# Performance work log

Hardware: AMD Instinct MI355X
Metric: run time of the kernel (lower is better)

Reference implementation:

```python
import jax, jax.numpy as jnp
import numpy as np

H = 1024  # hidden_size


def _cell(x, W, b):
    # x: [S, B, D_in]; W: [4H, D_in]; b: [4H]
    # One big batched matmul over all timesteps (no recurrence exists).
    gates = jnp.einsum('sbd,gd->sbg', x, W) + b  # [S, B, 4H]
    i, f, g, o = jnp.split(gates, 4, axis=-1)
    i = jax.nn.sigmoid(i)
    g = jnp.tanh(g)
    o = jax.nn.sigmoid(o)
    c = i * g
    h = o * jnp.tanh(c)
    return h, c


def setup_inputs() -> dict:
    key = jax.random.key(0)
    ks = jax.random.split(key, 9)
    S, B, D = 2048, 8, 1024
    s = 1.0 / np.sqrt(D)
    s2 = 1.0 / np.sqrt(2 * H)
    return {
        'x': jax.random.normal(ks[0], (S, B, D), dtype=jnp.float32),
        'W_f0': jax.random.uniform(ks[1], (4 * H, D), jnp.float32, -s, s),
        'b_f0': jax.random.uniform(ks[2], (4 * H,), jnp.float32, -s, s),
        'W_b0': jax.random.uniform(ks[3], (4 * H, D), jnp.float32, -s, s),
        'b_b0': jax.random.uniform(ks[4], (4 * H,), jnp.float32, -s, s),
        'W_f1': jax.random.uniform(ks[5], (4 * H, 2 * H), jnp.float32, -s2, s2),
        'b_f1': jax.random.uniform(ks[6], (4 * H,), jnp.float32, -s2, s2),
        'W_b1': jax.random.uniform(ks[7], (4 * H, 2 * H), jnp.float32, -s2, s2),
        'b_b1': jax.random.uniform(ks[8], (4 * H,), jnp.float32, -s2, s2),
    }


def reference(x, W_f0, b_f0, W_b0, b_b0, W_f1, b_f1, W_b1, b_b1):
    out = x
    h_ns, c_ns = [], []
    for (Wf, bf, Wb, bb) in [(W_f0, b_f0, W_b0, b_b0), (W_f1, b_f1, W_b1, b_b1)]:
        h_f, c_f = _cell(out, Wf, bf)  # forward direction
        h_b, c_b = _cell(out, Wb, bb)  # backward direction (same per-t math)
        out = jnp.concatenate([h_f, h_b], axis=-1)  # [S, B, 2H]
        # forward final state is at t = S-1; backward final state at t = 0
        h_ns += [h_f[-1], h_b[0]]
        c_ns += [c_f[-1], c_b[0]]
    h_n = jnp.stack(h_ns, axis=0)  # [num_layers*2, B, H]
    c_n = jnp.stack(c_ns, axis=0)
    return out, h_n, c_n
```

## Files before the change

### kernel.cpp

```cpp
#include <hip/hip_runtime.h>
#include <hip/hip_bf16.h>

#define S_LEN 2048
#define BATCH 8
#define HID   1024
#define NP    3072
#define MROWS 16384

using bf16x8 = __attribute__((ext_vector_type(8))) short;
using f32x4  = __attribute__((ext_vector_type(4))) float;

__device__ __forceinline__ unsigned short f2b(float f) {
  unsigned int u = __builtin_bit_cast(unsigned int, f);
  u += 0x7fffu + ((u >> 16) & 1u);
  return (unsigned short)(u >> 16);
}

__device__ __forceinline__ void load_lds16(const void* g, void* l) {
  __builtin_amdgcn_global_load_lds(
      (const __attribute__((address_space(1))) void*)g,
      (__attribute__((address_space(3))) void*)(unsigned int)(unsigned long long)l,
      16, 0, 0);
}

__global__ void cvt_f32_bf16(const float* __restrict__ in,
                             unsigned short* __restrict__ out, int n4) {
  int i = blockIdx.x * blockDim.x + threadIdx.x;
  if (i >= n4) return;
  const float4 v = reinterpret_cast<const float4*>(in)[i];
  ushort4 u;
  u.x = f2b(v.x); u.y = f2b(v.y); u.z = f2b(v.z); u.w = f2b(v.w);
  reinterpret_cast<ushort4*>(out)[i] = u;
}

__global__ void permute_w(const float* __restrict__ W,
                          unsigned short* __restrict__ Wp, int K) {
  long i = ((long)blockIdx.x * blockDim.x + threadIdx.x) * 4;
  int np = (int)(i / K);
  if (np >= NP) return;
  int k0 = (int)(i % K);
  int chunk = np / 48, rem = np % 48;
  int g3 = rem >> 4, hl = rem & 15;
  int og = (g3 == 0) ? 0 : (g3 == 1) ? 2 : 3;
  int n  = og * 1024 + chunk * 16 + hl;
  const float4 v = *reinterpret_cast<const float4*>(W + (long)n * K + k0);
  ushort4 u;
  u.x = f2b(v.x); u.y = f2b(v.y); u.z = f2b(v.z); u.w = f2b(v.w);
  *reinterpret_cast<ushort4*>(Wp + i) = u;
}

__global__ void permute_b(const float* __restrict__ b, float* __restrict__ bp) {
  int np = blockIdx.x * blockDim.x + threadIdx.x;
  if (np >= NP) return;
  int chunk = np / 48, rem = np % 48;
  int g3 = rem >> 4, hl = rem & 15;
  int og = (g3 == 0) ? 0 : (g3 == 1) ? 2 : 3;
  bp[np] = b[og * 1024 + chunk * 16 + hl];
}

template <int MODE>
__global__ void __launch_bounds__(256, 2)
lstm_gemm(const unsigned short* __restrict__ A,
          const unsigned short* __restrict__ WpF,
          const unsigned short* __restrict__ WpB,
          const float* __restrict__ bpF, const float* __restrict__ bpB,
          int K,
          unsigned short* __restrict__ out_bf, float* __restrict__ out_f,
          float* __restrict__ hn, float* __restrict__ cn) {
  const int dir = blockIdx.z;
  const unsigned short* __restrict__ Wp = dir ? WpB : WpF;
  const float* __restrict__ bp = dir ? bpB : bpF;
  const int bm = blockIdx.y;
  const int bn = blockIdx.x;

  __shared__ __align__(16) unsigned short Abuf[128 * 64];
  __shared__ __align__(16) unsigned short Bbuf[96 * 64];

  const int tid  = threadIdx.x;
  const int wid  = tid >> 6;
  const int lane = tid & 63;
  const int wm   = wid >> 1;
  const int wn   = wid & 1;

  f32x4 acc[4][3];
  const f32x4 zero = {0.f, 0.f, 0.f, 0.f};
#pragma unroll
  for (int i = 0; i < 4; ++i)
#pragma unroll
    for (int j = 0; j < 3; ++j) acc[i][j] = zero;

  const long a_base_row = (long)bm * 128;
  const long b_base_row = (long)bn * 96;
  const int  kt_count   = K >> 6;
  const long krow_bytes = (long)K * 2;

  for (int kt = 0; kt < kt_count; ++kt) {
    const long kbyte = (long)kt * 128;
#pragma unroll
    for (int it = 0; it < 4; ++it) {
      const int base = (it * 4 + wid) * 1024;
      const int p    = base + lane * 16;
      const int row  = p >> 7;
      const int colb = (p & 127) ^ ((row & 7) << 4);
      const char* src = (const char*)A + (a_base_row + row) * krow_bytes + kbyte + colb;
      load_lds16(src, (char*)Abuf + base);
    }
#pragma unroll
    for (int it = 0; it < 3; ++it) {
      const int base = (it * 4 + wid) * 1024;
      const int p    = base + lane * 16;
      const int row  = p >> 7;
      const int colb = (p & 127) ^ ((row & 7) << 4);
      const char* src = (const char*)Wp + (b_base_row + row) * krow_bytes + kbyte + colb;
      load_lds16(src, (char*)Bbuf + base);
    }
    asm volatile("s_waitcnt vmcnt(0)" ::: "memory");
    __syncthreads();

#pragma unroll
    for (int kb = 0; kb < 2; ++kb) {
      bf16x8 af[4];
      bf16x8 bfr[3];
#pragma unroll
      for (int mf = 0; mf < 4; ++mf) {
        const int row = wm * 64 + mf * 16 + (lane & 15);
        int byte = row * 128 + kb * 64 + ((lane >> 4) * 16);
        byte ^= (row & 7) << 4;
        af[mf] = *(const bf16x8*)((const char*)Abuf + byte);
      }
#pragma unroll
      for (int nf = 0; nf < 3; ++nf) {
        const int row = wn * 48 + nf * 16 + (lane & 15);
        int byte = row * 128 + kb * 64 + ((lane >> 4) * 16);
        byte ^= (row & 7) << 4;
        bfr[nf] = *(const bf16x8*)((const char*)Bbuf + byte);
      }
#pragma unroll
      for (int mf = 0; mf < 4; ++mf)
#pragma unroll
        for (int nf = 0; nf < 3; ++nf)
          acc[mf][nf] = __builtin_amdgcn_mfma_f32_16x16x32_bf16(
              af[mf], bfr[nf], acc[mf][nf], 0, 0, 0);
    }
    __syncthreads();
  }

  const int col    = lane & 15;
  const int chunk  = bn * 2 + wn;
  const int h      = chunk * 16 + col;
  const int outcol = dir * HID + h;
  const float bi = bp[chunk * 48 + col];
  const float bg = bp[chunk * 48 + 16 + col];
  const float bo = bp[chunk * 48 + 32 + col];
  const int Lidx = MODE * 2 + dir;

#pragma unroll
  for (int mf = 0; mf < 4; ++mf) {
#pragma unroll
    for (int r = 0; r < 4; ++r) {
      const int m = bm * 128 + wm * 64 + mf * 16 + (lane >> 4) * 4 + r;
      const float iv = acc[mf][0][r] + bi;
      const float gv = acc[mf][1][r] + bg;
      const float ov = acc[mf][2][r] + bo;
      const float is = 1.f / (1.f + __expf(-iv));
      const float gt = tanhf(gv);
      const float os = 1.f / (1.f + __expf(-ov));
      const float c  = is * gt;
      const float hv = os * tanhf(c);
      if (MODE == 0) {
        out_bf[(long)m * 2048 + outcol] = f2b(hv);
      } else {
        out_f[(long)m * 2048 + outcol] = hv;
      }
      const bool wst = (dir == 0) ? (m >= (S_LEN - 1) * BATCH) : (m < BATCH);
      if (wst) {
        const int b = (dir == 0) ? (m - (S_LEN - 1) * BATCH) : m;
        hn[((long)Lidx * BATCH + b) * HID + h] = hv;
        cn[((long)Lidx * BATCH + b) * HID + h] = c;
      }
    }
  }
}

extern "C" void kernel_launch(void* const* d_in, const int* in_sizes, int n_in,
                              void* d_out, int out_size, void* d_ws, size_t ws_size,
                              hipStream_t stream) {
  const float* x    = (const float*)d_in[0];
  const float* W_f0 = (const float*)d_in[1];
  const float* b_f0 = (const float*)d_in[2];
  const float* W_b0 = (const float*)d_in[3];
  const float* b_b0 = (const float*)d_in[4];
  const float* W_f1 = (const float*)d_in[5];
  const float* b_f1 = (const float*)d_in[6];
  const float* W_b1 = (const float*)d_in[7];
  const float* b_b1 = (const float*)d_in[8];

  float* out = (float*)d_out;
  float* hn  = out + (long)MROWS * 2048;
  float* cn  = hn + 4 * BATCH * HID;

  unsigned short* x_bf  = (unsigned short*)d_ws;
  unsigned short* out1  = x_bf + (long)MROWS * 1024;
  unsigned short* wp_f0 = out1 + (long)MROWS * 2048;
  unsigned short* wp_b0 = wp_f0 + (long)NP * 1024;
  unsigned short* wp_f1 = wp_b0 + (long)NP * 1024;
  unsigned short* wp_b1 = wp_f1 + (long)NP * 2048;
  float* bp_f0 = (float*)(wp_b1 + (long)NP * 2048);
  float* bp_b0 = bp_f0 + NP;
  float* bp_f1 = bp_b0 + NP;
  float* bp_b1 = bp_f1 + NP;

  cvt_f32_bf16<<<16384, 256, 0, stream>>>(x, x_bf, MROWS * 1024 / 4);
  permute_w<<<3072, 256, 0, stream>>>(W_f0, wp_f0, 1024);
  permute_w<<<3072, 256, 0, stream>>>(W_b0, wp_b0, 1024);
  permute_w<<<6144, 256, 0, stream>>>(W_f1, wp_f1, 2048);
  permute_w<<<6144, 256, 0, stream>>>(W_b1, wp_b1, 2048);
  permute_b<<<12, 256, 0, stream>>>(b_f0, bp_f0);
  permute_b<<<12, 256, 0, stream>>>(b_b0, bp_b0);
  permute_b<<<12, 256, 0, stream>>>(b_f1, bp_f1);
  permute_b<<<12, 256, 0, stream>>>(b_b1, bp_b1);

  dim3 grid(NP / 96, MROWS / 128, 2);
  lstm_gemm<0><<<grid, 256, 0, stream>>>(x_bf, wp_f0, wp_b0, bp_f0, bp_b0, 1024,
                                         out1, nullptr, hn, cn);
  lstm_gemm<1><<<grid, 256, 0, stream>>>(out1, wp_f1, wp_b1, bp_f1, bp_b1, 2048,
                                         nullptr, out, hn, cn);
}
```

Baseline: 666.3 us.

## Rewrite LSTM GEMM as 512-thread 128x384 tile with 4-stage LDS pipeline

The GEMM kernel moves from 256-thread 128x96 tiles with single-buffered LDS and a full vmcnt(0) wait each k-step to 512-thread 128x384 tiles. These use a 128KB LDS ring of four half-k stages, prefetched ahead with global_load_lds and interleaved with MFMA phases that raise wave priority via s_setprio. The goal is to hide global-load latency and increase reuse of each A tile across more gate columns. In exchange each block holds 24 accumulators per thread, uses many more barriers, and occupancy drops to about one block per CU because of the LDS footprint.

Measured after the change: 808.4 us. 1.21x slower.

```diff
diff --git a/kernel.cpp b/kernel.cpp
--- a/kernel.cpp
+++ b/kernel.cpp
@@ -22,6 +22,9 @@
       (__attribute__((address_space(3))) void*)(unsigned int)(unsigned long long)l,
       16, 0, 0);
 }
+
+#define MEMFENCE asm volatile("" ::: "memory")
+#define BARRIER  do { MEMFENCE; __builtin_amdgcn_s_barrier(); MEMFENCE; } while (0)
 
 __global__ void cvt_f32_bf16(const float* __restrict__ in,
                              unsigned short* __restrict__ out, int n4) {
@@ -59,7 +62,7 @@
 }
 
 template <int MODE>
-__global__ void __launch_bounds__(256, 2)
+__global__ void __launch_bounds__(512, 2)
 lstm_gemm(const unsigned short* __restrict__ A,
           const unsigned short* __restrict__ WpF,
           const unsigned short* __restrict__ WpB,
@@ -67,116 +70,150 @@
           int K,
           unsigned short* __restrict__ out_bf, float* __restrict__ out_f,
           float* __restrict__ hn, float* __restrict__ cn) {
+  __shared__ __align__(16) char lds[131072];
+
   const int dir = blockIdx.z;
   const unsigned short* __restrict__ Wp = dir ? WpB : WpF;
   const float* __restrict__ bp = dir ? bpB : bpF;
   const int bm = blockIdx.y;
   const int bn = blockIdx.x;
 
-  __shared__ __align__(16) unsigned short Abuf[128 * 64];
-  __shared__ __align__(16) unsigned short Bbuf[96 * 64];
-
   const int tid  = threadIdx.x;
   const int wid  = tid >> 6;
   const int lane = tid & 63;
-  const int wm   = wid >> 1;
-  const int wn   = wid & 1;
-
-  f32x4 acc[4][3];
+  const int wm   = wid >> 2;
+  const int wn   = wid & 3;
+
+  const int  nt = K >> 6;
+  const long K2 = (long)K * 2;
+
+  const int srow  = tid >> 3;
+  const int scolb = (((tid & 7) ^ (srow & 7)) << 4);
+  const char* Asrc = (const char*)A  + ((long)bm * 128 + srow) * K2 + scolb;
+  const char* Bsrc = (const char*)Wp + ((long)bn * 384 + srow) * K2 + scolb;
+  char* ldsw = lds + wid * 1024;
+
+  const int co0 = (((lane >> 4) << 4)) ^ ((lane & 7) << 4);
+  const int co1 = (64 + ((lane >> 4) << 4)) ^ ((lane & 7) << 4);
+  const int arow_off  = (lane & 15) * 128;
+  const int bbase_off = 8192 + (wn & 1) * 12288 + (lane & 15) * 128;
+
+  f32x4 acc[4][6];
   const f32x4 zero = {0.f, 0.f, 0.f, 0.f};
 #pragma unroll
   for (int i = 0; i < 4; ++i)
 #pragma unroll
-    for (int j = 0; j < 3; ++j) acc[i][j] = zero;
-
-  const long a_base_row = (long)bm * 128;
-  const long b_base_row = (long)bn * 96;
-  const int  kt_count   = K >> 6;
-  const long krow_bytes = (long)K * 2;
-
-  for (int kt = 0; kt < kt_count; ++kt) {
-    const long kbyte = (long)kt * 128;
-#pragma unroll
-    for (int it = 0; it < 4; ++it) {
-      const int base = (it * 4 + wid) * 1024;
-      const int p    = base + lane * 16;
-      const int row  = p >> 7;
-      const int colb = (p & 127) ^ ((row & 7) << 4);
-      const char* src = (const char*)A + (a_base_row + row) * krow_bytes + kbyte + colb;
-      load_lds16(src, (char*)Abuf + base);
+    for (int j = 0; j < 6; ++j) acc[i][j] = zero;
+
+  auto STAGE = [&](int s) {
+    if (s < 2 * nt) {
+      const long off = (long)(s >> 1) * 128;
+      const long h   = (long)(s & 1);
+      char* d = ldsw + (s & 3) * 32768;
+      load_lds16(Asrc + h * 64 * K2 + off,            d);
+      load_lds16(Bsrc + (h * 192      ) * K2 + off,   d + 8192);
+      load_lds16(Bsrc + (h * 192 +  64) * K2 + off,   d + 16384);
+      load_lds16(Bsrc + (h * 192 + 128) * K2 + off,   d + 24576);
     }
-#pragma unroll
-    for (int it = 0; it < 3; ++it) {
-      const int base = (it * 4 + wid) * 1024;
-      const int p    = base + lane * 16;
-      const int row  = p >> 7;
-      const int colb = (p & 127) ^ ((row & 7) << 4);
-      const char* src = (const char*)Wp + (b_base_row + row) * krow_bytes + kbyte + colb;
-      load_lds16(src, (char*)Bbuf + base);
+  };
+
+  STAGE(0); STAGE(1); STAGE(2); STAGE(3);
+  asm volatile("s_waitcnt vmcnt(8)" ::: "memory");
+  BARRIER;
+
+#define MFMA_ROW(mf, areg)                                                   \
+  do {                                                                       \
+    __builtin_amdgcn_s_setprio(1);                                           \
+    _Pragma("unroll")                                                        \
+    for (int nf = 0; nf < 6; ++nf) {                                         \
+      acc[mf][nf] = __builtin_amdgcn_mfma_f32_16x16x32_bf16(                 \
+          areg[0], b0[nf], acc[mf][nf], 0, 0, 0);                            \
+      acc[mf][nf] = __builtin_amdgcn_mfma_f32_16x16x32_bf16(                 \
+          areg[1], b1[nf], acc[mf][nf], 0, 0, 0);                            \
+    }                                                                        \
+    __builtin_amdgcn_s_setprio(0);                                           \
+  } while (0)
+
+  for (int t = 0; t < nt; ++t) {
+    const char* bufA = lds + ((2 * t + wm)        & 3) * 32768 + arow_off;
+    const char* bufB = lds + ((2 * t + (wn >> 1)) & 3) * 32768 + bbase_off;
+
+    bf16x8 b0[6], b1[6], a0[2], a1[2], a2[2], a3[2];
+
+#pragma unroll
+    for (int nf = 0; nf < 6; ++nf) {
+      b0[nf] = *(const bf16x8*)(bufB + nf * 2048 + co0);
+      b1[nf] = *(const bf16x8*)(bufB + nf * 2048 + co1);
     }
-    asm volatile("s_waitcnt vmcnt(0)" ::: "memory");
-    __syncthreads();
-
-#pragma unroll
-    for (int kb = 0; kb < 2; ++kb) {
-      bf16x8 af[4];
-      bf16x8 bfr[3];
-#pragma unroll
-      for (int mf = 0; mf < 4; ++mf) {
-        const int row = wm * 64 + mf * 16 + (lane & 15);
-        int byte = row * 128 + kb * 64 + ((lane >> 4) * 16);
-        byte ^= (row & 7) << 4;
-        af[mf] = *(const bf16x8*)((const char*)Abuf + byte);
-      }
-#pragma unroll
-      for (int nf = 0; nf < 3; ++nf) {
-        const int row = wn * 48 + nf * 16 + (lane & 15);
-        int byte = row * 128 + kb * 64 + ((lane >> 4) * 16);
-        byte ^= (row & 7) << 4;
-        bfr[nf] = *(const bf16x8*)((const char*)Bbuf + byte);
-      }
-#pragma unroll
-      for (int mf = 0; mf < 4; ++mf)
-#pragma unroll
-        for (int nf = 0; nf < 3; ++nf)
-          acc[mf][nf] = __builtin_amdgcn_mfma_f32_16x16x32_bf16(
-              af[mf], bfr[nf], acc[mf][nf], 0, 0, 0);
-    }
-    __syncthreads();
+    a0[0] = *(const bf16x8*)(bufA + co0);
+    a0[1] = *(const bf16x8*)(bufA + co1);
+    BARRIER;
+    asm volatile("s_waitcnt lgkmcnt(0)" ::: "memory");
+    MFMA_ROW(0, a0);
+    BARRIER;
+
+    a1[0] = *(const bf16x8*)(bufA + 2048 + co0);
+    a1[1] = *(const bf16x8*)(bufA + 2048 + co1);
+    a2[0] = *(const bf16x8*)(bufA + 4096 + co0);
+    a2[1] = *(const bf16x8*)(bufA + 4096 + co1);
+    a3[0] = *(const bf16x8*)(bufA + 6144 + co0);
+    a3[1] = *(const bf16x8*)(bufA + 6144 + co1);
+    BARRIER;
+    asm volatile("s_waitcnt lgkmcnt(0)" ::: "memory");
+    MFMA_ROW(1, a1);
+    BARRIER;
+
+    STAGE(2 * t + 4);
+    BARRIER;
+    MFMA_ROW(2, a2);
+    BARRIER;
+
+    STAGE(2 * t + 5);
+    BARRIER;
+    MFMA_ROW(3, a3);
+    if (t < nt - 2) { asm volatile("s_waitcnt vmcnt(8)" ::: "memory"); }
+    else            { asm volatile("s_waitcnt vmcnt(0)" ::: "memory"); }
+    BARRIER;
   }
+#undef MFMA_ROW
 
   const int col    = lane & 15;
-  const int chunk  = bn * 2 + wn;
-  const int h      = chunk * 16 + col;
-  const int outcol = dir * HID + h;
-  const float bi = bp[chunk * 48 + col];
-  const float bg = bp[chunk * 48 + 16 + col];
-  const float bo = bp[chunk * 48 + 32 + col];
-  const int Lidx = MODE * 2 + dir;
-
-#pragma unroll
-  for (int mf = 0; mf < 4; ++mf) {
-#pragma unroll
-    for (int r = 0; r < 4; ++r) {
-      const int m = bm * 128 + wm * 64 + mf * 16 + (lane >> 4) * 4 + r;
-      const float iv = acc[mf][0][r] + bi;
-      const float gv = acc[mf][1][r] + bg;
-      const float ov = acc[mf][2][r] + bo;
-      const float is = 1.f / (1.f + __expf(-iv));
-      const float gt = tanhf(gv);
-      const float os = 1.f / (1.f + __expf(-ov));
-      const float c  = is * gt;
-      const float hv = os * tanhf(c);
-      if (MODE == 0) {
-        out_bf[(long)m * 2048 + outcol] = f2b(hv);
-      } else {
-        out_f[(long)m * 2048 + outcol] = hv;
-      }
-      const bool wst = (dir == 0) ? (m >= (S_LEN - 1) * BATCH) : (m < BATCH);
-      if (wst) {
-        const int b = (dir == 0) ? (m - (S_LEN - 1) * BATCH) : m;
-        hn[((long)Lidx * BATCH + b) * HID + h] = hv;
-        cn[((long)Lidx * BATCH + b) * HID + h] = c;
+  const int rbase  = (lane >> 4) * 4;
+  const int chunk0 = bn * 8 + wn * 2;
+  const int Lidx   = MODE * 2 + dir;
+
+#pragma unroll
+  for (int hg = 0; hg < 2; ++hg) {
+    const int chunk  = chunk0 + hg;
+    const int h      = chunk * 16 + col;
+    const int outcol = dir * HID + h;
+    const float bi = bp[chunk * 48 + col];
+    const float bg = bp[chunk * 48 + 16 + col];
+    const float bo = bp[chunk * 48 + 32 + col];
+#pragma unroll
+    for (int mf = 0; mf < 4; ++mf) {
+#pragma unroll
+      for (int r = 0; r < 4; ++r) {
+        const int m = bm * 128 + wm * 64 + mf * 16 + rbase + r;
+        const float iv = acc[mf][hg * 3 + 0][r] + bi;
+        const float gv = acc[mf][hg * 3 + 1][r] + bg;
+        const float ov = acc[mf][hg * 3 + 2][r] + bo;
+        const float is = 1.f / (1.f + __expf(-iv));
+        const float gt = tanhf(gv);
+        const float os = 1.f / (1.f + __expf(-ov));
+        const float c  = is * gt;
+        const float hv = os * tanhf(c);
+        if (MODE == 0) {
+          out_bf[(long)m * 2048 + outcol] = f2b(hv);
+        } else {
+          out_f[(long)m * 2048 + outcol] = hv;
+        }
+        const bool wst = (dir == 0) ? (m >= (S_LEN - 1) * BATCH) : (m < BATCH);
+        if (wst) {
+          const int b = (dir == 0) ? (m - (S_LEN - 1) * BATCH) : m;
+          hn[((long)Lidx * BATCH + b) * HID + h] = hv;
+          cn[((long)Lidx * BATCH + b) * HID + h] = c;
+        }
       }
     }
   }
@@ -220,9 +257,9 @@
   permute_b<<<12, 256, 0, stream>>>(b_f1, bp_f1);
   permute_b<<<12, 256, 0, stream>>>(b_b1, bp_b1);
 
-  dim3 grid(NP / 96, MROWS / 128, 2);
-  lstm_gemm<0><<<grid, 256, 0, stream>>>(x_bf, wp_f0, wp_b0, bp_f0, bp_b0, 1024,
+  dim3 grid(NP / 384, MROWS / 128, 2);
+  lstm_gemm<0><<<grid, 512, 0, stream>>>(x_bf, wp_f0, wp_b0, bp_f0, bp_b0, 1024,
                                          out1, nullptr, hn, cn);
-  lstm_gemm<1><<<grid, 256, 0, stream>>>(out1, wp_f1, wp_b1, bp_f1, bp_b1, 2048,
+  lstm_gemm<1><<<grid, 512, 0, stream>>>(out1, wp_f1, wp_b1, bp_f1, bp_b1, 2048,
                                          nullptr, out, hn, cn);
 }
```

## Double-buffer LDS tiles and widen GEMM N-tile to 192 columns

Applied to the files above, without the earlier changes.

The fused LSTM GEMM kernel now uses two LDS stages, so global-to-LDS loads for the next K tile are issued while MFMAs run on the current one, with one barrier per iteration instead of two. The block N-tile doubles from 96 to 192, so each wave holds 4x6 accumulators and covers two gate chunks, which raises A-tile reuse. MFMA issue is wrapped in s_setprio. In exchange, LDS use grows to 80 KB and register pressure rises, which can limit occupancy below the two-blocks-per-CU launch bound.

Result: no change. 657.0 us (-1.4%).

```diff
diff --git a/kernel.cpp b/kernel.cpp
--- a/kernel.cpp
+++ b/kernel.cpp
@@ -22,6 +22,9 @@
       (__attribute__((address_space(3))) void*)(unsigned int)(unsigned long long)l,
       16, 0, 0);
 }
+
+#define MEMFENCE asm volatile("" ::: "memory")
+#define BARRIER  do { MEMFENCE; __builtin_amdgcn_s_barrier(); MEMFENCE; } while (0)
 
 __global__ void cvt_f32_bf16(const float* __restrict__ in,
                              unsigned short* __restrict__ out, int n4) {
@@ -67,116 +70,130 @@
           int K,
           unsigned short* __restrict__ out_bf, float* __restrict__ out_f,
           float* __restrict__ hn, float* __restrict__ cn) {
+  __shared__ __align__(16) char lds[81920];
+
   const int dir = blockIdx.z;
   const unsigned short* __restrict__ Wp = dir ? WpB : WpF;
   const float* __restrict__ bp = dir ? bpB : bpF;
   const int bm = blockIdx.y;
   const int bn = blockIdx.x;
 
-  __shared__ __align__(16) unsigned short Abuf[128 * 64];
-  __shared__ __align__(16) unsigned short Bbuf[96 * 64];
-
   const int tid  = threadIdx.x;
   const int wid  = tid >> 6;
   const int lane = tid & 63;
   const int wm   = wid >> 1;
   const int wn   = wid & 1;
 
-  f32x4 acc[4][3];
+  const int  nt = K >> 6;
+  const long K2 = (long)K * 2;
+
+  const int rlane = lane >> 3;
+  const int cb    = (((lane & 7) ^ rlane) << 4);
+  const char* Asrc = (const char*)A  + ((long)bm * 128 + rlane) * K2 + cb;
+  const char* Bsrc = (const char*)Wp + ((long)bn * 192 + rlane) * K2 + cb;
+
+  const int l15 = lane & 15;
+  const int hi  = lane >> 4;
+  const int c0  = ((hi ^ (l15 & 7)) << 4);
+  const int aro = (wm * 64 + l15) * 128;
+  const int bro = 16384 + (wn * 96 + l15) * 128;
+
+  f32x4 acc[4][6];
   const f32x4 zero = {0.f, 0.f, 0.f, 0.f};
 #pragma unroll
   for (int i = 0; i < 4; ++i)
 #pragma unroll
-    for (int j = 0; j < 3; ++j) acc[i][j] = zero;
-
-  const long a_base_row = (long)bm * 128;
-  const long b_base_row = (long)bn * 96;
-  const int  kt_count   = K >> 6;
-  const long krow_bytes = (long)K * 2;
-
-  for (int kt = 0; kt < kt_count; ++kt) {
-    const long kbyte = (long)kt * 128;
-#pragma unroll
-    for (int it = 0; it < 4; ++it) {
-      const int base = (it * 4 + wid) * 1024;
-      const int p    = base + lane * 16;
-      const int row  = p >> 7;
-      const int colb = (p & 127) ^ ((row & 7) << 4);
-      const char* src = (const char*)A + (a_base_row + row) * krow_bytes + kbyte + colb;
-      load_lds16(src, (char*)Abuf + base);
-    }
-#pragma unroll
-    for (int it = 0; it < 3; ++it) {
-      const int base = (it * 4 + wid) * 1024;
-      const int p    = base + lane * 16;
-      const int row  = p >> 7;
-      const int colb = (p & 127) ^ ((row & 7) << 4);
-      const char* src = (const char*)Wp + (b_base_row + row) * krow_bytes + kbyte + colb;
-      load_lds16(src, (char*)Bbuf + base);
-    }
+    for (int j = 0; j < 6; ++j) acc[i][j] = zero;
+
+  auto STAGE = [&](int t) {
+    if (t >= nt) return;
+    char* d = lds + (t & 1) * 40960;
+    const long off = (long)t * 128;
+#pragma unroll
+    for (int s = 0; s < 4; ++s) {
+      const int slot = s * 4 + wid;
+      load_lds16(Asrc + (long)(slot * 8) * K2 + off, d + slot * 1024);
+    }
+#pragma unroll
+    for (int s = 0; s < 6; ++s) {
+      const int slot = s * 4 + wid;
+      load_lds16(Bsrc + (long)(slot * 8) * K2 + off, d + 16384 + slot * 1024);
+    }
+  };
+
+  STAGE(0);
+  asm volatile("s_waitcnt vmcnt(0)" ::: "memory");
+  BARRIER;
+
+  for (int t = 0; t < nt; ++t) {
+    STAGE(t + 1);
+
+    const char* buf = lds + (t & 1) * 40960;
+    bf16x8 a[4][2], b[6][2];
+#pragma unroll
+    for (int nf = 0; nf < 6; ++nf) {
+      b[nf][0] = *(const bf16x8*)(buf + bro + nf * 2048 + c0);
+      b[nf][1] = *(const bf16x8*)(buf + bro + nf * 2048 + (c0 ^ 64));
+    }
+#pragma unroll
+    for (int mf = 0; mf < 4; ++mf) {
+      a[mf][0] = *(const bf16x8*)(buf + aro + mf * 2048 + c0);
+      a[mf][1] = *(const bf16x8*)(buf + aro + mf * 2048 + (c0 ^ 64));
+    }
+
+    __builtin_amdgcn_s_setprio(1);
+#pragma unroll
+    for (int mf = 0; mf < 4; ++mf)
+#pragma unroll
+      for (int nf = 0; nf < 6; ++nf) {
+        acc[mf][nf] = __builtin_amdgcn_mfma_f32_16x16x32_bf16(
+            a[mf][0], b[nf][0], acc[mf][nf], 0, 0, 0);
+        acc[mf][nf] = __builtin_amdgcn_mfma_f32_16x16x32_bf16(
+            a[mf][1], b[nf][1], acc[mf][nf], 0, 0, 0);
+      }
+    __builtin_amdgcn_s_setprio(0);
+
     asm volatile("s_waitcnt vmcnt(0)" ::: "memory");
-    __syncthreads();
-
-#pragma unroll
-    for (int kb = 0; kb < 2; ++kb) {
-      bf16x8 af[4];
-      bf16x8 bfr[3];
-#pragma unroll
-      for (int mf = 0; mf < 4; ++mf) {
-        const int row = wm * 64 + mf * 16 + (lane & 15);
-        int byte = row * 128 + kb * 64 + ((lane >> 4) * 16);
-        byte ^= (row & 7) << 4;
-        af[mf] = *(const bf16x8*)((const char*)Abuf + byte);
-      }
-#pragma unroll
-      for (int nf = 0; nf < 3; ++nf) {
-        const int row = wn * 48 + nf * 16 + (lane & 15);
-        int byte = row * 128 + kb * 64 + ((lane >> 4) * 16);
-        byte ^= (row & 7) << 4;
-        bfr[nf] = *(const bf16x8*)((const char*)Bbuf + byte);
-      }
-#pragma unroll
-      for (int mf = 0; mf < 4; ++mf)
-#pragma unroll
-        for (int nf = 0; nf < 3; ++nf)
-          acc[mf][nf] = __builtin_amdgcn_mfma_f32_16x16x32_bf16(
-              af[mf], bfr[nf], acc[mf][nf], 0, 0, 0);
-    }
-    __syncthreads();
+    BARRIER;
   }
 
-  const int col    = lane & 15;
-  const int chunk  = bn * 2 + wn;
-  const int h      = chunk * 16 + col;
-  const int outcol = dir * HID + h;
-  const float bi = bp[chunk * 48 + col];
-  const float bg = bp[chunk * 48 + 16 + col];
-  const float bo = bp[chunk * 48 + 32 + col];
-  const int Lidx = MODE * 2 + dir;
-
-#pragma unroll
-  for (int mf = 0; mf < 4; ++mf) {
-#pragma unroll
-    for (int r = 0; r < 4; ++r) {
-      const int m = bm * 128 + wm * 64 + mf * 16 + (lane >> 4) * 4 + r;
-      const float iv = acc[mf][0][r] + bi;
-      const float gv = acc[mf][1][r] + bg;
-      const float ov = acc[mf][2][r] + bo;
-      const float is = 1.f / (1.f + __expf(-iv));
-      const float gt = tanhf(gv);
-      const float os = 1.f / (1.f + __expf(-ov));
-      const float c  = is * gt;
-      const float hv = os * tanhf(c);
-      if (MODE == 0) {
-        out_bf[(long)m * 2048 + outcol] = f2b(hv);
-      } else {
-        out_f[(long)m * 2048 + outcol] = hv;
-      }
-      const bool wst = (dir == 0) ? (m >= (S_LEN - 1) * BATCH) : (m < BATCH);
-      if (wst) {
-        const int b = (dir == 0) ? (m - (S_LEN - 1) * BATCH) : m;
-        hn[((long)Lidx * BATCH + b) * HID + h] = hv;
-        cn[((long)Lidx * BATCH + b) * HID + h] = c;
+  const int col    = l15;
+  const int rbase  = hi * 4;
+  const int chunk0 = bn * 4 + wn * 2;
+  const int Lidx   = MODE * 2 + dir;
+
+#pragma unroll
+  for (int hg = 0; hg < 2; ++hg) {
+    const int chunk  = chunk0 + hg;
+    const int h      = chunk * 16 + col;
+    const int outcol = dir * HID + h;
+    const float bi = bp[chunk * 48 + col];
+    const float bg = bp[chunk * 48 + 16 + col];
+    const float bo = bp[chunk * 48 + 32 + col];
+#pragma unroll
+    for (int mf = 0; mf < 4; ++mf) {
+#pragma unroll
+      for (int r = 0; r < 4; ++r) {
+        const int m = bm * 128 + wm * 64 + mf * 16 + rbase + r;
+        const float iv = acc[mf][hg * 3 + 0][r] + bi;
+        const float gv = acc[mf][hg * 3 + 1][r] + bg;
+        const float ov = acc[mf][hg * 3 + 2][r] + bo;
+        const float is = 1.f / (1.f + __expf(-iv));
+        const float gt = tanhf(gv);
+        const float os = 1.f / (1.f + __expf(-ov));
+        const float c  = is * gt;
+        const float hv = os * tanhf(c);
+        if (MODE == 0) {
+          out_bf[(long)m * 2048 + outcol] = f2b(hv);
+        } else {
+          out_f[(long)m * 2048 + outcol] = hv;
+        }
+        const bool wst = (dir == 0) ? (m >= (S_LEN - 1) * BATCH) : (m < BATCH);
+        if (wst) {
+          const int b = (dir == 0) ? (m - (S_LEN - 1) * BATCH) : m;
+          hn[((long)Lidx * BATCH + b) * HID + h] = hv;
+          cn[((long)Lidx * BATCH + b) * HID + h] = c;
+        }
       }
     }
   }
@@ -220,7 +237,7 @@
   permute_b<<<12, 256, 0, stream>>>(b_f1, bp_f1);
   permute_b<<<12, 256, 0, stream>>>(b_b1, bp_b1);
 
-  dim3 grid(NP / 96, MROWS / 128, 2);
+  dim3 grid(NP / 192, MROWS / 128, 2);
   lstm_gemm<0><<<grid, 256, 0, stream>>>(x_bf, wp_f0, wp_b0, bp_f0, bp_b0, 1024,
                                          out1, nullptr, hn, cn);
   lstm_gemm<1><<<grid, 256, 0, stream>>>(out1, wp_f1, wp_b1, bp_f1, bp_b1, 2048,
```

## Enlarge GEMM tiles to 256x384 with 32x32 MFMA and triple-buffered LDS pipeline

Applied to the files above, without the earlier changes.

Rewrites the fused LSTM GEMM so each 512-thread block computes a 256x384 tile with 32x32x16 bf16 MFMAs. Loads for k-step t+2 are issued into a triple-buffered LDS ring while step t computes, using partial vmcnt waits in place of a full drain. Weights and bias are re-permuted into 32-wide gate chunks to match, and tanh is replaced with an exp-based form. The goal is more data reuse per loaded byte and load latency hidden behind compute, at the cost of 120KB LDS per block (one block per CU), fewer blocks overall, and higher register pressure.

Measured after the change: 739.5 us. 1.11x slower.

```diff
diff --git a/kernel.cpp b/kernel.cpp
--- a/kernel.cpp
+++ b/kernel.cpp
@@ -8,12 +8,19 @@
 #define MROWS 16384
 
 using bf16x8 = __attribute__((ext_vector_type(8))) short;
-using f32x4  = __attribute__((ext_vector_type(4))) float;
+using f32x16 = __attribute__((ext_vector_type(16))) float;
 
 __device__ __forceinline__ unsigned short f2b(float f) {
   unsigned int u = __builtin_bit_cast(unsigned int, f);
   u += 0x7fffu + ((u >> 16) & 1u);
   return (unsigned short)(u >> 16);
+}
+
+__device__ __forceinline__ float sigf(float x) {
+  return 1.f / (1.f + __expf(-x));
+}
+__device__ __forceinline__ float tanh_f(float x) {
+  return 2.f / (1.f + __expf(-2.f * x)) - 1.f;
 }
 
 __device__ __forceinline__ void load_lds16(const void* g, void* l) {
@@ -22,6 +29,9 @@
       (__attribute__((address_space(3))) void*)(unsigned int)(unsigned long long)l,
       16, 0, 0);
 }
+
+#define MEMFENCE asm volatile("" ::: "memory")
+#define BARRIER  do { MEMFENCE; __builtin_amdgcn_s_barrier(); MEMFENCE; } while (0)
 
 __global__ void cvt_f32_bf16(const float* __restrict__ in,
                              unsigned short* __restrict__ out, int n4) {
@@ -39,10 +49,10 @@
   int np = (int)(i / K);
   if (np >= NP) return;
   int k0 = (int)(i % K);
-  int chunk = np / 48, rem = np % 48;
-  int g3 = rem >> 4, hl = rem & 15;
-  int og = (g3 == 0) ? 0 : (g3 == 1) ? 2 : 3;
-  int n  = og * 1024 + chunk * 16 + hl;
+  int c32 = np / 96, rem = np % 96;
+  int gate = rem >> 5, hl = rem & 31;
+  int og = (gate == 0) ? 0 : (gate == 1) ? 2 : 3;
+  int n  = og * 1024 + c32 * 32 + hl;
   const float4 v = *reinterpret_cast<const float4*>(W + (long)n * K + k0);
   ushort4 u;
   u.x = f2b(v.x); u.y = f2b(v.y); u.z = f2b(v.z); u.w = f2b(v.w);
@@ -52,14 +62,17 @@
 __global__ void permute_b(const float* __restrict__ b, float* __restrict__ bp) {
   int np = blockIdx.x * blockDim.x + threadIdx.x;
   if (np >= NP) return;
-  int chunk = np / 48, rem = np % 48;
-  int g3 = rem >> 4, hl = rem & 15;
-  int og = (g3 == 0) ? 0 : (g3 == 1) ? 2 : 3;
-  bp[np] = b[og * 1024 + chunk * 16 + hl];
-}
+  int c32 = np / 96, rem = np % 96;
+  int gate = rem >> 5, hl = rem & 31;
+  int og = (gate == 0) ? 0 : (gate == 1) ? 2 : 3;
+  bp[np] = b[og * 1024 + c32 * 32 + hl];
+}
+
+#define MFMAOP(a_, b_, c_) \
+  c_ = __builtin_amdgcn_mfma_f32_32x32x16_bf16(a_, b_, c_, 0, 0, 0)
 
 template <int MODE>
-__global__ void __launch_bounds__(256, 2)
+__global__ void __launch_bounds__(512, 2)
 lstm_gemm(const unsigned short* __restrict__ A,
           const unsigned short* __restrict__ WpF,
           const unsigned short* __restrict__ WpB,
@@ -67,106 +80,142 @@
           int K,
           unsigned short* __restrict__ out_bf, float* __restrict__ out_f,
           float* __restrict__ hn, float* __restrict__ cn) {
+  __shared__ __align__(16) char lds[122880];
+
   const int dir = blockIdx.z;
   const unsigned short* __restrict__ Wp = dir ? WpB : WpF;
   const float* __restrict__ bp = dir ? bpB : bpF;
   const int bm = blockIdx.y;
   const int bn = blockIdx.x;
 
-  __shared__ __align__(16) unsigned short Abuf[128 * 64];
-  __shared__ __align__(16) unsigned short Bbuf[96 * 64];
-
   const int tid  = threadIdx.x;
   const int wid  = tid >> 6;
   const int lane = tid & 63;
-  const int wm   = wid >> 1;
-  const int wn   = wid & 1;
-
-  f32x4 acc[4][3];
-  const f32x4 zero = {0.f, 0.f, 0.f, 0.f};
+  const int wm   = wid >> 2;
+  const int wn   = wid & 3;
+
+  const int  nt = K >> 5;
+  const long K2 = (long)K * 2;
+
+  const int lls = lane >> 3;
+  const int phs = lane & 7;
+  const char *s0, *s1, *s2, *s3, *s4;
+  int d0, d1, d2, d3, d4;
+#define MKSLICE(j, SRC, DD) do {                                   \
+    const int sl = wid + 8 * (j);                                  \
+    if (sl < 16) {                                    \
+      const int line = sl * 8 + lls;                               \
+      const int lg   = phs ^ (line & 7);                           \
+      const long grow = (long)bm * 256 + line * 2 + (lg >> 2);     \
+      SRC = (const char*)A + grow * K2 + (lg & 3) * 16;            \
+      DD  = sl * 1024;                                             \
+    } else {                                          \
+      const int jb = sl - 16;                                      \
+      const int line = jb * 8 + lls;                               \
+      const int lg   = phs ^ (line & 7);                           \
+      const long grow = (long)bn * 384 + line * 2 + (lg >> 2);     \
+      SRC = (const char*)Wp + grow * K2 + (lg & 3) * 16;           \
+      DD  = 16384 + jb * 1024;                                     \
+    }                                                              \
+  } while (0)
+  MKSLICE(0, s0, d0); MKSLICE(1, s1, d1); MKSLICE(2, s2, d2);
+  MKSLICE(3, s3, d3); MKSLICE(4, s4, d4);
+#undef MKSLICE
+
+#define ISSUE(T, DB) do {                                          \
+    const long ko_ = (long)(T) * 64;                               \
+    load_lds16(s0 + ko_, (DB) + d0);                               \
+    load_lds16(s1 + ko_, (DB) + d1);                               \
+    load_lds16(s2 + ko_, (DB) + d2);                               \
+    load_lds16(s3 + ko_, (DB) + d3);                               \
+    load_lds16(s4 + ko_, (DB) + d4);                               \
+  } while (0)
+
+  const int l31 = lane & 31;
+  const int b5  = lane >> 5;
+  auto frag_off = [&](int row) {
+    const int line = row >> 1;
+    const int lg   = (row & 1) * 4 + b5;
+    return line * 128 + ((lg ^ (line & 7)) * 16);
+  };
+  const int a0o = frag_off(wm * 128 + 0  + l31);
+  const int a1o = frag_off(wm * 128 + 32 + l31);
+  const int a2o = frag_off(wm * 128 + 64 + l31);
+  const int a3o = frag_off(wm * 128 + 96 + l31);
+  const int b0o = 16384 + frag_off(wn * 96 + 0  + l31);
+  const int b1o = 16384 + frag_off(wn * 96 + 32 + l31);
+  const int b2o = 16384 + frag_off(wn * 96 + 64 + l31);
+
+  f32x16 acc[4][3];
 #pragma unroll
   for (int i = 0; i < 4; ++i)
 #pragma unroll
-    for (int j = 0; j < 3; ++j) acc[i][j] = zero;
-
-  const long a_base_row = (long)bm * 128;
-  const long b_base_row = (long)bn * 96;
-  const int  kt_count   = K >> 6;
-  const long krow_bytes = (long)K * 2;
-
-  for (int kt = 0; kt < kt_count; ++kt) {
-    const long kbyte = (long)kt * 128;
-#pragma unroll
-    for (int it = 0; it < 4; ++it) {
-      const int base = (it * 4 + wid) * 1024;
-      const int p    = base + lane * 16;
-      const int row  = p >> 7;
-      const int colb = (p & 127) ^ ((row & 7) << 4);
-      const char* src = (const char*)A + (a_base_row + row) * krow_bytes + kbyte + colb;
-      load_lds16(src, (char*)Abuf + base);
-    }
-#pragma unroll
-    for (int it = 0; it < 3; ++it) {
-      const int base = (it * 4 + wid) * 1024;
-      const int p    = base + lane * 16;
-      const int row  = p >> 7;
-      const int colb = (p & 127) ^ ((row & 7) << 4);
-      const char* src = (const char*)Wp + (b_base_row + row) * krow_bytes + kbyte + colb;
-      load_lds16(src, (char*)Bbuf + base);
-    }
-    asm volatile("s_waitcnt vmcnt(0)" ::: "memory");
-    __syncthreads();
-
-#pragma unroll
-    for (int kb = 0; kb < 2; ++kb) {
-      bf16x8 af[4];
-      bf16x8 bfr[3];
-#pragma unroll
-      for (int mf = 0; mf < 4; ++mf) {
-        const int row = wm * 64 + mf * 16 + (lane & 15);
-        int byte = row * 128 + kb * 64 + ((lane >> 4) * 16);
-        byte ^= (row & 7) << 4;
-        af[mf] = *(const bf16x8*)((const char*)Abuf + byte);
-      }
-#pragma unroll
-      for (int nf = 0; nf < 3; ++nf) {
-        const int row = wn * 48 + nf * 16 + (lane & 15);
-        int byte = row * 128 + kb * 64 + ((lane >> 4) * 16);
-        byte ^= (row & 7) << 4;
-        bfr[nf] = *(const bf16x8*)((const char*)Bbuf + byte);
-      }
-#pragma unroll
-      for (int mf = 0; mf < 4; ++mf)
-#pragma unroll
-        for (int nf = 0; nf < 3; ++nf)
-          acc[mf][nf] = __builtin_amdgcn_mfma_f32_16x16x32_bf16(
-              af[mf], bfr[nf], acc[mf][nf], 0, 0, 0);
-    }
-    __syncthreads();
+    for (int j = 0; j < 3; ++j)
+      acc[i][j] = (f32x16)(0.f);
+
+  char* p0 = lds;
+  char* p1 = lds + 40960;
+  char* p2 = lds + 81920;
+
+  ISSUE(0, p0); MEMFENCE;
+  ISSUE(1, p1); MEMFENCE;
+  asm volatile("s_waitcnt vmcnt(5)" ::: "memory");
+  BARRIER;
+
+#define KSTEP(X) do {                                              \
+    bf16x8 A0 = *(const bf16x8*)(p0 + (a0o ^ (X)));                \
+    bf16x8 A1 = *(const bf16x8*)(p0 + (a1o ^ (X)));                \
+    bf16x8 A2 = *(const bf16x8*)(p0 + (a2o ^ (X)));                \
+    bf16x8 A3 = *(const bf16x8*)(p0 + (a3o ^ (X)));                \
+    bf16x8 B0 = *(const bf16x8*)(p0 + (b0o ^ (X)));                \
+    bf16x8 B1 = *(const bf16x8*)(p0 + (b1o ^ (X)));                \
+    bf16x8 B2 = *(const bf16x8*)(p0 + (b2o ^ (X)));                \
+    __builtin_amdgcn_s_setprio(1);                                 \
+    MFMAOP(A0, B0, acc[0][0]); MFMAOP(A1, B0, acc[1][0]);          \
+    MFMAOP(A2, B0, acc[2][0]); MFMAOP(A3, B0, acc[3][0]);          \
+    MFMAOP(A0, B1, acc[0][1]); MFMAOP(A1, B1, acc[1][1]);          \
+    MFMAOP(A2, B1, acc[2][1]); MFMAOP(A3, B1, acc[3][1]);          \
+    MFMAOP(A0, B2, acc[0][2]); MFMAOP(A1, B2, acc[1][2]);          \
+    MFMAOP(A2, B2, acc[2][2]); MFMAOP(A3, B2, acc[3][2]);          \
+    __builtin_amdgcn_s_setprio(0);                                 \
+  } while (0)
+
+#pragma unroll 1
+  for (int t = 0; t < nt; ++t) {
+    if (t + 2 < nt) { ISSUE(t + 2, p2); }
+    MEMFENCE;
+    KSTEP(0);
+    KSTEP(32);
+    if (t < nt - 2) { asm volatile("s_waitcnt vmcnt(5)" ::: "memory"); }
+    else            { asm volatile("s_waitcnt vmcnt(0)" ::: "memory"); }
+    BARRIER;
+    char* tp = p0; p0 = p1; p1 = p2; p2 = tp;
   }
-
-  const int col    = lane & 15;
-  const int chunk  = bn * 2 + wn;
-  const int h      = chunk * 16 + col;
+#undef KSTEP
+#undef ISSUE
+
+  const int c32  = bn * 4 + wn;
+  const int h    = c32 * 32 + l31;
   const int outcol = dir * HID + h;
-  const float bi = bp[chunk * 48 + col];
-  const float bg = bp[chunk * 48 + 16 + col];
-  const float bo = bp[chunk * 48 + 32 + col];
+  const float bi = bp[c32 * 96 + l31];
+  const float bg = bp[c32 * 96 + 32 + l31];
+  const float bo = bp[c32 * 96 + 64 + l31];
   const int Lidx = MODE * 2 + dir;
+  const int mrow0 = bm * 256 + wm * 128 + b5 * 4;
 
 #pragma unroll
   for (int mf = 0; mf < 4; ++mf) {
 #pragma unroll
-    for (int r = 0; r < 4; ++r) {
-      const int m = bm * 128 + wm * 64 + mf * 16 + (lane >> 4) * 4 + r;
+    for (int r = 0; r < 16; ++r) {
+      const int m = mrow0 + mf * 32 + (r & 3) + 8 * (r >> 2);
       const float iv = acc[mf][0][r] + bi;
       const float gv = acc[mf][1][r] + bg;
       const float ov = acc[mf][2][r] + bo;
-      const float is = 1.f / (1.f + __expf(-iv));
-      const float gt = tanhf(gv);
-      const float os = 1.f / (1.f + __expf(-ov));
+      const float is = sigf(iv);
+      const float gt = tanh_f(gv);
+      const float os = sigf(ov);
       const float c  = is * gt;
-      const float hv = os * tanhf(c);
+      const float hv = os * tanh_f(c);
       if (MODE == 0) {
         out_bf[(long)m * 2048 + outcol] = f2b(hv);
       } else {
@@ -220,9 +269,9 @@
   permute_b<<<12, 256, 0, stream>>>(b_f1, bp_f1);
   permute_b<<<12, 256, 0, stream>>>(b_b1, bp_b1);
 
-  dim3 grid(NP / 96, MROWS / 128, 2);
-  lstm_gemm<0><<<grid, 256, 0, stream>>>(x_bf, wp_f0, wp_b0, bp_f0, bp_b0, 1024,
+  dim3 grid(NP / 384, MROWS / 256, 2);
+  lstm_gemm<0><<<grid, 512, 0, stream>>>(x_bf, wp_f0, wp_b0, bp_f0, bp_b0, 1024,
                                          out1, nullptr, hn, cn);
-  lstm_gemm<1><<<grid, 256, 0, stream>>>(out1, wp_f1, wp_b1, bp_f1, bp_b1, 2048,
+  lstm_gemm<1><<<grid, 512, 0, stream>>>(out1, wp_f1, wp_b1, bp_f1, bp_b1, 2048,
                                          nullptr, out, hn, cn);
 }
```
